# Optimization experiments

Hardware: AMD Instinct MI355X
Metric: run time of the kernel (lower is better)

The kernel has to match this reference:

```python
import jax, jax.numpy as jnp
import numpy as np

B, S, E, H = 2, 2048, 1024, 16
D = E // H  # head_dim = 64


def setup_inputs() -> dict:
    key = jax.random.key(0)
    ks = jax.random.split(key, 5)
    return {
        "hidden_states": jax.random.normal(ks[0], (B, S, E), jnp.float32),
        "c_attn_w": jax.random.normal(ks[1], (E, 3 * E), jnp.float32) * 0.02,
        "c_attn_b": jnp.zeros((3 * E,), jnp.float32),
        "c_proj_w": jax.random.normal(ks[2], (E, E), jnp.float32) * 0.02,
        "c_proj_b": jnp.zeros((E,), jnp.float32),
    }


def reference(hidden_states, c_attn_w, c_attn_b, c_proj_w, c_proj_b):
    # Conv1D: x @ w + b -> qkv [B, S, 3E]
    qkv = hidden_states @ c_attn_w + c_attn_b
    q, k, v = jnp.split(qkv, 3, axis=-1)
    # [B, H, S, D]
    q = q.reshape(B, S, H, D).transpose(0, 2, 1, 3)
    k = k.reshape(B, S, H, D).transpose(0, 2, 1, 3)
    v = v.reshape(B, S, H, D).transpose(0, 2, 1, 3)
    # scores [B, H, S, S], scaled by sqrt(head_dim)
    scores = jnp.einsum("bhqd,bhkd->bhqk", q, k) / jnp.sqrt(jnp.asarray(D, q.dtype))
    causal = jnp.tril(jnp.ones((S, S), bool))  # [S, S]
    mask_value = jnp.finfo(scores.dtype).min
    scores = jnp.where(causal, scores, mask_value)
    attn = jax.nn.softmax(scores, axis=-1)
    # attn @ V -> [B, H, S, D] -> [B, S, E]
    out = jnp.einsum("bhqk,bhkd->bhqd", attn, v)
    out = out.transpose(0, 2, 1, 3).reshape(B, S, E)
    return out @ c_proj_w + c_proj_b
```

## Files before the change

kernel.cpp:

```cpp
#include <hip/hip_runtime.h>

using bf16 = __bf16;
typedef __bf16 bf16x8 __attribute__((ext_vector_type(8)));
typedef __bf16 bf16x4 __attribute__((ext_vector_type(4)));
typedef float  f32x4  __attribute__((ext_vector_type(4)));

#define MFMA16(a, b, c) __builtin_amdgcn_mfma_f32_16x16x32_bf16((a), (b), (c), 0, 0, 0)

static constexpr int S = 2048, E = 1024;
static constexpr float CSCALE = 0.18033688011112042f;

__device__ __forceinline__ void gld16(const bf16* g, bf16* l) {
    __builtin_amdgcn_global_load_lds((const __attribute__((address_space(1))) unsigned*)g,
                                     (__attribute__((address_space(3))) unsigned*)l, 16, 0, 0);
}

__global__ __launch_bounds__(256) void k_prep(const float* __restrict__ hs, const float* __restrict__ w0,
                                              const float* __restrict__ w1, bf16* __restrict__ A0,
                                              bf16* __restrict__ Wt0, bf16* __restrict__ Wt1) {
    __shared__ float tile[32][33];
    const int bx = blockIdx.x;
    if (bx < 4096) {
        int i = (bx * 256 + threadIdx.x) * 4;
        float4 v = *(const float4*)(hs + i);
        bf16x4 o = { (bf16)v.x, (bf16)v.y, (bf16)v.z, (bf16)v.w };
        *(bf16x4*)(A0 + i) = o;
        return;
    }
    const float* in;
    bf16* outp;
    int K, N, nb, kb;
    if (bx < 4096 + 3072) {
        int j = bx - 4096; in = w0; outp = Wt0; K = 1024; N = 3072; nb = j % 96; kb = j / 96;
    } else {
        int j = bx - 7168; in = w1; outp = Wt1; K = 1024; N = 1024; nb = j % 32; kb = j / 32;
    }
    const int bxx = nb * 32, byy = kb * 32;
    const int tx = threadIdx.x & 31, ty = threadIdx.x >> 5;
#pragma unroll
    for (int i = 0; i < 32; i += 8)
        tile[ty + i][tx] = in[(long)(byy + ty + i) * N + bxx + tx];
    __syncthreads();
#pragma unroll
    for (int i = 0; i < 32; i += 8)
        outp[(long)(bxx + ty + i) * K + byy + tx] = (bf16)tile[tx][ty + i];
}

__global__ __launch_bounds__(256) void k_gemm_qkv(const bf16* __restrict__ A, const bf16* __restrict__ Bt,
                                                  const float* __restrict__ bias, bf16* __restrict__ Qs,
                                                  bf16* __restrict__ Kf, bf16* __restrict__ Vf, int Kk) {
    const int bm = blockIdx.x * 128;
    const int bn = blockIdx.y * 128;
    const int tid = threadIdx.x;
    const int w = tid >> 6, lane = tid & 63;
    const int wm = (w >> 1) * 64, wn = (w & 1) * 64;
    const int col = lane & 15, quad = lane >> 4;

    __shared__ __align__(16) char smem[32768];
    bf16* sA = (bf16*)smem;
    bf16* sB = (bf16*)(smem + 16384);
    bf16* T  = (bf16*)smem;

    const bf16* pA[4]; const bf16* pB[4]; bf16* lA[4]; bf16* lB[4];
#pragma unroll
    for (int i = 0; i < 4; i++) {
        const int c = i * 256 + w * 64 + lane;
        const int r = c >> 3, sl = (c & 7) ^ (r & 7);
        pA[i] = A  + (long)(bm + r) * Kk + sl * 8;
        pB[i] = Bt + (long)(bn + r) * Kk + sl * 8;
        lA[i] = sA + i * 2048 + w * 512;
        lB[i] = sB + i * 2048 + w * 512;
    }

    f32x4 acc[4][4] = {};

    for (int k0 = 0; k0 < Kk; k0 += 64) {
        __syncthreads();
#pragma unroll
        for (int i = 0; i < 4; i++) gld16(pA[i] + k0, lA[i]);
#pragma unroll
        for (int i = 0; i < 4; i++) gld16(pB[i] + k0, lB[i]);
        __syncthreads();
#pragma unroll
        for (int h = 0; h < 2; h++) {
            bf16x8 af[4], bfr[4];
#pragma unroll
            for (int mt = 0; mt < 4; mt++) {
                const int row = wm + mt * 16 + col;
                af[mt] = *(const bf16x8*)(sA + row * 64 + (((h * 4 + quad) ^ (col & 7)) * 8));
            }
#pragma unroll
            for (int nt = 0; nt < 4; nt++) {
                const int row = wn + nt * 16 + col;
                bfr[nt] = *(const bf16x8*)(sB + row * 64 + (((h * 4 + quad) ^ (col & 7)) * 8));
            }
#pragma unroll
            for (int mt = 0; mt < 4; mt++)
#pragma unroll
                for (int nt = 0; nt < 4; nt++)
                    acc[mt][nt] = MFMA16(af[mt], bfr[nt], acc[mt][nt]);
        }
    }

    const int seg = bn >> 10;
    const int b = bm >> 11;
    const int kt0 = (bm & 2047) >> 6;

    if (seg == 0) {
#pragma unroll
        for (int mt = 0; mt < 4; mt++) {
            const int gr = bm + wm + mt * 16 + quad * 4;
#pragma unroll
            for (int nt = 0; nt < 4; nt++) {
                const int gc = bn + wn + nt * 16 + col;
                const float bv = bias[gc];
#pragma unroll
                for (int r = 0; r < 4; r++)
                    Qs[(long)(gr + r) * 1024 + gc] = (bf16)((acc[mt][nt][r] + bv) * CSCALE);
            }
        }
        return;
    }

    const int hl = w >> 1;
    if (seg == 1) {
        const int bh = b * 16 + (bn >> 6) - 16 + hl;
#pragma unroll 1
        for (int p = 0; p < 2; p++) {
            __syncthreads();
            if ((wm >> 6) == p) {
#pragma unroll
                for (int mt = 0; mt < 4; mt++) {
                    const int sl = mt * 16 + quad * 4;
#pragma unroll
                    for (int nt = 0; nt < 4; nt++) {
                        const int gcl = wn + nt * 16 + col;
                        const float bv = bias[bn + gcl];
#pragma unroll
                        for (int r = 0; r < 4; r++)
                            T[(sl + r) * 136 + gcl] = (bf16)(acc[mt][nt][r] + bv);
                    }
                }
            }
            __syncthreads();
            const int ktp = kt0 + p;
#pragma unroll
            for (int mi = 0; mi < 2; mi++) {
                const int mt = (w & 1) * 2 + mi;
#pragma unroll
                for (int half = 0; half < 2; half++) {
                    bf16x8 ch = *(const bf16x8*)(T + (mt * 16 + col) * 136 + hl * 64 + half * 32 + quad * 8);
                    const long chunk = ((long)(bh * 32 + ktp) * 8 + mt * 2 + half) * 64 + lane;
                    *(bf16x8*)(Kf + chunk * 8) = ch;
                }
            }
        }
    } else {
        const int bh = b * 16 + (bn >> 6) - 32 + hl;
#pragma unroll 1
        for (int p = 0; p < 2; p++) {
            __syncthreads();
            if ((wm >> 6) == p) {
#pragma unroll
                for (int mt = 0; mt < 4; mt++) {
                    const int sl = mt * 16 + quad * 4;
#pragma unroll
                    for (int nt = 0; nt < 4; nt++) {
                        const int gcl = wn + nt * 16 + col;
                        const float bv = bias[bn + gcl];
                        bf16x4 pk = { (bf16)(acc[mt][nt][0] + bv), (bf16)(acc[mt][nt][1] + bv),
                                      (bf16)(acc[mt][nt][2] + bv), (bf16)(acc[mt][nt][3] + bv) };
                        *(bf16x4*)(T + gcl * 72 + sl) = pk;
                    }
                }
            }
            __syncthreads();
            const int ktp = kt0 + p;
#pragma unroll
            for (int di = 0; di < 2; di++) {
                const int dt = (w & 1) * 2 + di;
#pragma unroll
                for (int ks = 0; ks < 2; ks++) {
                    bf16x8 ch = *(const bf16x8*)(T + (hl * 64 + dt * 16 + col) * 72 + ks * 32 + quad * 8);
                    const long chunk = ((long)(bh * 32 + ktp) * 8 + dt * 2 + ks) * 64 + lane;
                    *(bf16x8*)(Vf + chunk * 8) = ch;
                }
            }
        }
    }
}

__global__ __launch_bounds__(256) void k_gemm_bt64(const bf16* __restrict__ A, const bf16* __restrict__ Bt,
                                                    const float* __restrict__ bias, float* __restrict__ Cout,
                                                    int Mm, int Nn, int Kk) {
    const int bm = blockIdx.x * 64;
    const int bn = blockIdx.y * 128;
    const int tid = threadIdx.x;
    const int w = tid >> 6, lane = tid & 63;
    const int wm = (w >> 1) * 32, wn = (w & 1) * 64;
    const int col = lane & 15, quad = lane >> 4;

    __shared__ bf16 sA[64 * 64];
    __shared__ bf16 sB[128 * 64];

    const bf16* pA[2]; bf16* lA[2];
#pragma unroll
    for (int i = 0; i < 2; i++) {
        const int c = i * 256 + w * 64 + lane;
        const int r = c >> 3, sl = (c & 7) ^ (r & 7);
        pA[i] = A + (long)(bm + r) * Kk + sl * 8;
        lA[i] = sA + i * 2048 + w * 512;
    }
    const bf16* pB[4]; bf16* lB[4];
#pragma unroll
    for (int i = 0; i < 4; i++) {
        const int c = i * 256 + w * 64 + lane;
        const int r = c >> 3, sl = (c & 7) ^ (r & 7);
        pB[i] = Bt + (long)(bn + r) * Kk + sl * 8;
        lB[i] = sB + i * 2048 + w * 512;
    }

    f32x4 acc[2][4] = {};

    for (int k0 = 0; k0 < Kk; k0 += 64) {
        __syncthreads();
#pragma unroll
        for (int i = 0; i < 2; i++) gld16(pA[i] + k0, lA[i]);
#pragma unroll
        for (int i = 0; i < 4; i++) gld16(pB[i] + k0, lB[i]);
        __syncthreads();
#pragma unroll
        for (int h = 0; h < 2; h++) {
            bf16x8 af[2], bfr[4];
#pragma unroll
            for (int mt = 0; mt < 2; mt++) {
                const int row = wm + mt * 16 + col;
                af[mt] = *(const bf16x8*)(sA + row * 64 + (((h * 4 + quad) ^ (col & 7)) * 8));
            }
#pragma unroll
            for (int nt = 0; nt < 4; nt++) {
                const int row = wn + nt * 16 + col;
                bfr[nt] = *(const bf16x8*)(sB + row * 64 + (((h * 4 + quad) ^ (col & 7)) * 8));
            }
#pragma unroll
            for (int mt = 0; mt < 2; mt++)
#pragma unroll
                for (int nt = 0; nt < 4; nt++)
                    acc[mt][nt] = MFMA16(af[mt], bfr[nt], acc[mt][nt]);
        }
    }

#pragma unroll
    for (int mt = 0; mt < 2; mt++) {
        const int gr = bm + wm + mt * 16 + quad * 4;
#pragma unroll
        for (int nt = 0; nt < 4; nt++) {
            const int gc = bn + wn + nt * 16 + col;
            const float bv = bias[gc];
#pragma unroll
            for (int r = 0; r < 4; r++)
                Cout[(long)(gr + r) * Nn + gc] = acc[mt][nt][r] + bv;
        }
    }
}

__global__ __launch_bounds__(512) void k_attn(const bf16* __restrict__ Qs, const bf16* __restrict__ Kf,
                                              const bf16* __restrict__ Vf, bf16* __restrict__ out) {
    const int bh = blockIdx.x & 31, g = blockIdx.x >> 5;
    const int b = bh >> 4, h = bh & 15;
    const int tid = threadIdx.x;
    const int w = tid >> 6, lane = tid & 63;
    const int col = lane & 15, quad = lane >> 4;
    const int wid = g * 4 + (w & 3);
    const int t = (w < 4) ? (63 - wid) : wid;
    const int q0 = t * 32;
    const int nkt = (t >> 1) + 1;

    __shared__ bf16 sP[8][32 * 72];
    bf16* pw = sP[w];

    const bf16* kfb = Kf + ((long)bh << 17) + lane * 8;
    const bf16* vfb = Vf + ((long)bh << 17) + lane * 8;

    bf16x8 bq[2][2];
#pragma unroll
    for (int qg = 0; qg < 2; qg++) {
        const bf16* qp = Qs + (long)(b * S + q0 + qg * 16 + col) * E + h * 64 + quad * 8;
        bq[qg][0] = *(const bf16x8*)(qp);
        bq[qg][1] = *(const bf16x8*)(qp + 32);
    }
    float m_[2] = { -1e30f, -1e30f }, l_[2] = { 0.f, 0.f };
    f32x4 o[2][4] = {};

#pragma unroll 1
    for (int kt = 0; kt < nkt; kt++) {
        bf16x8 kfr[4][2], vfr[4][2];
#pragma unroll
        for (int mt = 0; mt < 4; mt++)
#pragma unroll
            for (int half = 0; half < 2; half++)
                kfr[mt][half] = *(const bf16x8*)(kfb + ((long)(kt * 8 + mt * 2 + half) << 9));
#pragma unroll
        for (int dt = 0; dt < 4; dt++)
#pragma unroll
            for (int ks = 0; ks < 2; ks++)
                vfr[dt][ks] = *(const bf16x8*)(vfb + ((long)(kt * 8 + dt * 2 + ks) << 9));

        f32x4 s[2][4];
#pragma unroll
        for (int mt = 0; mt < 4; mt++)
#pragma unroll
            for (int qg = 0; qg < 2; qg++) {
                f32x4 z = {};
                z = MFMA16(kfr[mt][0], bq[qg][0], z);
                z = MFMA16(kfr[mt][1], bq[qg][1], z);
                s[qg][mt] = z;
            }
        if (kt == nkt - 1) {
#pragma unroll
            for (int qg = 0; qg < 2; qg++) {
                const int qrow = q0 + qg * 16 + col;
#pragma unroll
                for (int mt = 0; mt < 4; mt++)
#pragma unroll
                    for (int r = 0; r < 4; r++)
                        if (kt * 64 + mt * 16 + quad * 4 + r > qrow) s[qg][mt][r] = -1e30f;
            }
        }
#pragma unroll
        for (int qg = 0; qg < 2; qg++) {
            float cm = -1e30f;
#pragma unroll
            for (int mt = 0; mt < 4; mt++)
#pragma unroll
                for (int r = 0; r < 4; r++) cm = fmaxf(cm, s[qg][mt][r]);
            cm = fmaxf(cm, __shfl_xor(cm, 16));
            cm = fmaxf(cm, __shfl_xor(cm, 32));
            const float mnew = fmaxf(m_[qg], cm);
            const float alpha = __builtin_amdgcn_exp2f(m_[qg] - mnew);
            m_[qg] = mnew;
            float rs = 0.f;
#pragma unroll
            for (int mt = 0; mt < 4; mt++)
#pragma unroll
                for (int r = 0; r < 4; r++) {
                    float pe = __builtin_amdgcn_exp2f(s[qg][mt][r] - mnew);
                    s[qg][mt][r] = pe;
                    rs += pe;
                }
            l_[qg] = l_[qg] * alpha + rs;
#pragma unroll
            for (int dt = 0; dt < 4; dt++)
#pragma unroll
                for (int r = 0; r < 4; r++) o[qg][dt][r] *= alpha;
#pragma unroll
            for (int mt = 0; mt < 4; mt++) {
                bf16x4 pk = { (bf16)s[qg][mt][0], (bf16)s[qg][mt][1],
                              (bf16)s[qg][mt][2], (bf16)s[qg][mt][3] };
                *(bf16x4*)(pw + (qg * 16 + col) * 72 + mt * 16 + quad * 4) = pk;
            }
        }
#pragma unroll
        for (int ks = 0; ks < 2; ks++) {
            bf16x8 ap[2];
#pragma unroll
            for (int qg = 0; qg < 2; qg++)
                ap[qg] = *(const bf16x8*)(pw + (qg * 16 + col) * 72 + ks * 32 + quad * 8);
#pragma unroll
            for (int dt = 0; dt < 4; dt++)
#pragma unroll
                for (int qg = 0; qg < 2; qg++)
                    o[qg][dt] = MFMA16(vfr[dt][ks], ap[qg], o[qg][dt]);
        }
    }

#pragma unroll
    for (int qg = 0; qg < 2; qg++) {
        float lt = l_[qg];
        lt += __shfl_xor(lt, 16);
        lt += __shfl_xor(lt, 32);
        const float li = 1.f / lt;
        bf16* op = out + (long)(b * S + q0 + qg * 16 + col) * E + h * 64 + quad * 4;
#pragma unroll
        for (int dt = 0; dt < 4; dt++) {
            bf16x4 ov = { (bf16)(o[qg][dt][0] * li), (bf16)(o[qg][dt][1] * li),
                          (bf16)(o[qg][dt][2] * li), (bf16)(o[qg][dt][3] * li) };
            *(bf16x4*)(op + dt * 16) = ov;
        }
    }
}

extern "C" void kernel_launch(void* const* d_in, const int* in_sizes, int n_in,
                              void* d_out, int out_size, void* d_ws, size_t ws_size,
                              hipStream_t stream) {
    const float* hs = (const float*)d_in[0];
    const float* w0 = (const float*)d_in[1];
    const float* b0 = (const float*)d_in[2];
    const float* w1 = (const float*)d_in[3];
    const float* b1 = (const float*)d_in[4];
    float* outp = (float*)d_out;

    char* ws = (char*)d_ws;
    bf16* A0    = (bf16*)(ws);
    bf16* Wt0   = (bf16*)(ws + 8388608);
    bf16* Wt1   = (bf16*)(ws + 14680064);
    bf16* Qs    = (bf16*)(ws + 16777216);
    bf16* Kf    = (bf16*)(ws + 25165824);
    bf16* Vf    = (bf16*)(ws + 33554432);
    bf16* attnO = (bf16*)(ws + 41943040);

    k_prep<<<8192, 256, 0, stream>>>(hs, w0, w1, A0, Wt0, Wt1);
    k_gemm_qkv<<<dim3(32, 24), 256, 0, stream>>>(A0, Wt0, b0, Qs, Kf, Vf, 1024);
    k_attn<<<256, 512, 0, stream>>>(Qs, Kf, Vf, attnO);
    k_gemm_bt64<<<dim3(64, 8), 256, 0, stream>>>(attnO, Wt1, b1, outp, 4096, 1024, 1024);
}
```

Measured before the change: 182.8 us.

## Split attention KV range across two waves and merge partial softmax states

Restructures the attention kernel so each 128-thread block handles a complementary pair of 32-row query tiles, and within each tile the two waves split the key range in half (split-K flash attention). Wave 0 writes its partial output, max and sum to shared memory, and wave 1 merges them with rescaling before writing. This halves the serial key-loop length per wave to cut the critical path and raises the block count for better CU load balance. In exchange it adds a shared-memory merge, a block barrier per tile, and duplicated Q loads.

```diff
diff --git a/kernel.cpp b/kernel.cpp
--- a/kernel.cpp
+++ b/kernel.cpp
@@ -264,128 +264,162 @@
     }
 }
 
-__global__ __launch_bounds__(512) void k_attn(const bf16* __restrict__ Qs, const bf16* __restrict__ Kf,
+__global__ __launch_bounds__(128) void k_attn(const bf16* __restrict__ Qs, const bf16* __restrict__ Kf,
                                               const bf16* __restrict__ Vf, bf16* __restrict__ out) {
-    const int bh = blockIdx.x & 31, g = blockIdx.x >> 5;
+    const int bh = blockIdx.x & 31;
+    const int tp = blockIdx.x >> 5;
     const int b = bh >> 4, h = bh & 15;
     const int tid = threadIdx.x;
     const int w = tid >> 6, lane = tid & 63;
     const int col = lane & 15, quad = lane >> 4;
-    const int wid = g * 4 + (w & 3);
-    const int t = (w < 4) ? (63 - wid) : wid;
-    const int q0 = t * 32;
-    const int nkt = (t >> 1) + 1;
-
-    __shared__ bf16 sP[8][32 * 72];
+
+    __shared__ bf16 sP[2][32 * 72];
+    __shared__ float M[2][64][36];
     bf16* pw = sP[w];
 
     const bf16* kfb = Kf + ((long)bh << 17) + lane * 8;
     const bf16* vfb = Vf + ((long)bh << 17) + lane * 8;
 
-    bf16x8 bq[2][2];
-#pragma unroll
-    for (int qg = 0; qg < 2; qg++) {
-        const bf16* qp = Qs + (long)(b * S + q0 + qg * 16 + col) * E + h * 64 + quad * 8;
-        bq[qg][0] = *(const bf16x8*)(qp);
-        bq[qg][1] = *(const bf16x8*)(qp + 32);
-    }
-    float m_[2] = { -1e30f, -1e30f }, l_[2] = { 0.f, 0.f };
-    f32x4 o[2][4] = {};
-
 #pragma unroll 1
-    for (int kt = 0; kt < nkt; kt++) {
-        bf16x8 kfr[4][2], vfr[4][2];
-#pragma unroll
-        for (int mt = 0; mt < 4; mt++)
-#pragma unroll
-            for (int half = 0; half < 2; half++)
-                kfr[mt][half] = *(const bf16x8*)(kfb + ((long)(kt * 8 + mt * 2 + half) << 9));
-#pragma unroll
-        for (int dt = 0; dt < 4; dt++)
-#pragma unroll
-            for (int ks = 0; ks < 2; ks++)
-                vfr[dt][ks] = *(const bf16x8*)(vfb + ((long)(kt * 8 + dt * 2 + ks) << 9));
-
-        f32x4 s[2][4];
-#pragma unroll
-        for (int mt = 0; mt < 4; mt++)
+    for (int sel = 0; sel < 2; sel++) {
+        const int t = sel ? 63 - tp : tp;
+        const int q0 = t * 32;
+        const int nkt = (t >> 1) + 1;
+        const int kA = nkt >> 1;
+        const int kbeg = w ? kA : 0;
+        const int kend = w ? nkt : kA;
+
+        bf16x8 bq[2][2];
+#pragma unroll
+        for (int qg = 0; qg < 2; qg++) {
+            const bf16* qp = Qs + (long)(b * S + q0 + qg * 16 + col) * E + h * 64 + quad * 8;
+            bq[qg][0] = *(const bf16x8*)(qp);
+            bq[qg][1] = *(const bf16x8*)(qp + 32);
+        }
+        float m_[2] = { -1e30f, -1e30f }, l_[2] = { 0.f, 0.f };
+        f32x4 o[2][4] = {};
+
+#pragma unroll 1
+        for (int kt = kbeg; kt < kend; kt++) {
+            bf16x8 kfr[4][2], vfr[4][2];
+#pragma unroll
+            for (int mt = 0; mt < 4; mt++)
+#pragma unroll
+                for (int half = 0; half < 2; half++)
+                    kfr[mt][half] = *(const bf16x8*)(kfb + ((long)(kt * 8 + mt * 2 + half) << 9));
+#pragma unroll
+            for (int dt = 0; dt < 4; dt++)
+#pragma unroll
+                for (int ks = 0; ks < 2; ks++)
+                    vfr[dt][ks] = *(const bf16x8*)(vfb + ((long)(kt * 8 + dt * 2 + ks) << 9));
+
+            f32x4 s[2][4];
+#pragma unroll
+            for (int mt = 0; mt < 4; mt++)
+#pragma unroll
+                for (int qg = 0; qg < 2; qg++) {
+                    f32x4 z = {};
+                    z = MFMA16(kfr[mt][0], bq[qg][0], z);
+                    z = MFMA16(kfr[mt][1], bq[qg][1], z);
+                    s[qg][mt] = z;
+                }
+            if (kt == nkt - 1) {
+#pragma unroll
+                for (int qg = 0; qg < 2; qg++) {
+                    const int qrow = q0 + qg * 16 + col;
+#pragma unroll
+                    for (int mt = 0; mt < 4; mt++)
+#pragma unroll
+                        for (int r = 0; r < 4; r++)
+                            if (kt * 64 + mt * 16 + quad * 4 + r > qrow) s[qg][mt][r] = -1e30f;
+                }
+            }
 #pragma unroll
             for (int qg = 0; qg < 2; qg++) {
-                f32x4 z = {};
-                z = MFMA16(kfr[mt][0], bq[qg][0], z);
-                z = MFMA16(kfr[mt][1], bq[qg][1], z);
-                s[qg][mt] = z;
-            }
-        if (kt == nkt - 1) {
+                float cm = -1e30f;
+#pragma unroll
+                for (int mt = 0; mt < 4; mt++)
+#pragma unroll
+                    for (int r = 0; r < 4; r++) cm = fmaxf(cm, s[qg][mt][r]);
+                cm = fmaxf(cm, __shfl_xor(cm, 16));
+                cm = fmaxf(cm, __shfl_xor(cm, 32));
+                const float mnew = fmaxf(m_[qg], cm);
+                const float alpha = __builtin_amdgcn_exp2f(m_[qg] - mnew);
+                m_[qg] = mnew;
+                float rs = 0.f;
+#pragma unroll
+                for (int mt = 0; mt < 4; mt++)
+#pragma unroll
+                    for (int r = 0; r < 4; r++) {
+                        float pe = __builtin_amdgcn_exp2f(s[qg][mt][r] - mnew);
+                        s[qg][mt][r] = pe;
+                        rs += pe;
+                    }
+                l_[qg] = l_[qg] * alpha + rs;
+#pragma unroll
+                for (int dt = 0; dt < 4; dt++)
+#pragma unroll
+                    for (int r = 0; r < 4; r++) o[qg][dt][r] *= alpha;
+#pragma unroll
+                for (int mt = 0; mt < 4; mt++) {
+                    bf16x4 pk = { (bf16)s[qg][mt][0], (bf16)s[qg][mt][1],
+                                  (bf16)s[qg][mt][2], (bf16)s[qg][mt][3] };
+                    *(bf16x4*)(pw + (qg * 16 + col) * 72 + mt * 16 + quad * 4) = pk;
+                }
+            }
+#pragma unroll
+            for (int ks = 0; ks < 2; ks++) {
+                bf16x8 ap[2];
+#pragma unroll
+                for (int qg = 0; qg < 2; qg++)
+                    ap[qg] = *(const bf16x8*)(pw + (qg * 16 + col) * 72 + ks * 32 + quad * 8);
+#pragma unroll
+                for (int dt = 0; dt < 4; dt++)
+#pragma unroll
+                    for (int qg = 0; qg < 2; qg++)
+                        o[qg][dt] = MFMA16(vfr[dt][ks], ap[qg], o[qg][dt]);
+            }
+        }
+
+#pragma unroll
+        for (int qg = 0; qg < 2; qg++) {
+            float lt = l_[qg];
+            lt += __shfl_xor(lt, 16);
+            lt += __shfl_xor(lt, 32);
+            l_[qg] = lt;
+        }
+
+        if (w == 0) {
 #pragma unroll
             for (int qg = 0; qg < 2; qg++) {
-                const int qrow = q0 + qg * 16 + col;
-#pragma unroll
-                for (int mt = 0; mt < 4; mt++)
+#pragma unroll
+                for (int dt = 0; dt < 4; dt++)
+                    *(f32x4*)&M[sel][lane][qg * 16 + dt * 4] = o[qg][dt];
+                M[sel][lane][32 + qg * 2] = m_[qg];
+                M[sel][lane][33 + qg * 2] = l_[qg];
+            }
+        }
+        __syncthreads();
+        if (w == 1) {
+#pragma unroll
+            for (int qg = 0; qg < 2; qg++) {
+                const float m0 = M[sel][lane][32 + qg * 2];
+                const float l0 = M[sel][lane][33 + qg * 2];
+                const float mm = fmaxf(m0, m_[qg]);
+                const float a0 = __builtin_amdgcn_exp2f(m0 - mm);
+                const float a1 = __builtin_amdgcn_exp2f(m_[qg] - mm);
+                const float li = 1.f / (l0 * a0 + l_[qg] * a1);
+                bf16* op = out + (long)(b * S + q0 + qg * 16 + col) * E + h * 64 + quad * 4;
+#pragma unroll
+                for (int dt = 0; dt < 4; dt++) {
+                    f32x4 o0 = *(const f32x4*)&M[sel][lane][qg * 16 + dt * 4];
+                    bf16x4 ov;
 #pragma unroll
                     for (int r = 0; r < 4; r++)
-                        if (kt * 64 + mt * 16 + quad * 4 + r > qrow) s[qg][mt][r] = -1e30f;
-            }
-        }
-#pragma unroll
-        for (int qg = 0; qg < 2; qg++) {
-            float cm = -1e30f;
-#pragma unroll
-            for (int mt = 0; mt < 4; mt++)
-#pragma unroll
-                for (int r = 0; r < 4; r++) cm = fmaxf(cm, s[qg][mt][r]);
-            cm = fmaxf(cm, __shfl_xor(cm, 16));
-            cm = fmaxf(cm, __shfl_xor(cm, 32));
-            const float mnew = fmaxf(m_[qg], cm);
-            const float alpha = __builtin_amdgcn_exp2f(m_[qg] - mnew);
-            m_[qg] = mnew;
-            float rs = 0.f;
-#pragma unroll
-            for (int mt = 0; mt < 4; mt++)
-#pragma unroll
-                for (int r = 0; r < 4; r++) {
-                    float pe = __builtin_amdgcn_exp2f(s[qg][mt][r] - mnew);
-                    s[qg][mt][r] = pe;
-                    rs += pe;
-                }
-            l_[qg] = l_[qg] * alpha + rs;
-#pragma unroll
-            for (int dt = 0; dt < 4; dt++)
-#pragma unroll
-                for (int r = 0; r < 4; r++) o[qg][dt][r] *= alpha;
-#pragma unroll
-            for (int mt = 0; mt < 4; mt++) {
-                bf16x4 pk = { (bf16)s[qg][mt][0], (bf16)s[qg][mt][1],
-                              (bf16)s[qg][mt][2], (bf16)s[qg][mt][3] };
-                *(bf16x4*)(pw + (qg * 16 + col) * 72 + mt * 16 + quad * 4) = pk;
-            }
-        }
-#pragma unroll
-        for (int ks = 0; ks < 2; ks++) {
-            bf16x8 ap[2];
-#pragma unroll
-            for (int qg = 0; qg < 2; qg++)
-                ap[qg] = *(const bf16x8*)(pw + (qg * 16 + col) * 72 + ks * 32 + quad * 8);
-#pragma unroll
-            for (int dt = 0; dt < 4; dt++)
-#pragma unroll
-                for (int qg = 0; qg < 2; qg++)
-                    o[qg][dt] = MFMA16(vfr[dt][ks], ap[qg], o[qg][dt]);
-        }
-    }
-
-#pragma unroll
-    for (int qg = 0; qg < 2; qg++) {
-        float lt = l_[qg];
-        lt += __shfl_xor(lt, 16);
-        lt += __shfl_xor(lt, 32);
-        const float li = 1.f / lt;
-        bf16* op = out + (long)(b * S + q0 + qg * 16 + col) * E + h * 64 + quad * 4;
-#pragma unroll
-        for (int dt = 0; dt < 4; dt++) {
-            bf16x4 ov = { (bf16)(o[qg][dt][0] * li), (bf16)(o[qg][dt][1] * li),
-                          (bf16)(o[qg][dt][2] * li), (bf16)(o[qg][dt][3] * li) };
-            *(bf16x4*)(op + dt * 16) = ov;
+                        ov[r] = (bf16)((o0[r] * a0 + o[qg][dt][r] * a1) * li);
+                    *(bf16x4*)(op + dt * 16) = ov;
+                }
+            }
         }
     }
 }
@@ -411,6 +445,6 @@
 
     k_prep<<<8192, 256, 0, stream>>>(hs, w0, w1, A0, Wt0, Wt1);
     k_gemm_qkv<<<dim3(32, 24), 256, 0, stream>>>(A0, Wt0, b0, Qs, Kf, Vf, 1024);
-    k_attn<<<256, 512, 0, stream>>>(Qs, Kf, Vf, attnO);
+    k_attn<<<1024, 128, 0, stream>>>(Qs, Kf, Vf, attnO);
     k_gemm_bt64<<<dim3(64, 8), 256, 0, stream>>>(attnO, Wt1, b1, outp, 4096, 1024, 1024);
 }
```

After: 178.5 us. 1.02x faster.
